# Performance work log

Measured on AMD Instinct MI355X. Metric: run time of the kernel, lower is better.

The kernel has to match this reference:

```python
import jax, jax.numpy as jnp
import numpy as np

VALUES_PER_ITEM = 4  # 2-bit packed -> 4 values per uint8


def setup_inputs() -> dict:
    key = jax.random.key(0)
    k1, k2, k3 = jax.random.split(key, 3)
    x = jax.random.normal(k1, (4, 4096, 2048), dtype=jnp.float32)
    # packed uint8 weights, stored as int32 with values in [0, 256)
    weight_packed = jax.random.randint(k2, (512, 2048), 0, 256, dtype=jnp.int32)
    weight_scale = jnp.ones((1,), dtype=jnp.float32)
    bias = jax.random.normal(k3, (2048,), dtype=jnp.float32) * 0.01
    return {"x": x, "weight_packed": weight_packed,
            "weight_scale": weight_scale, "bias": bias}


def unpack_weights_bitnet(packed, dtype):
    # packed: [out//4, in]. HF BitNet layout: group i occupies rows
    # [i*out//4 : (i+1)*out//4], extracted from bits (2i, 2i+1), minus 1.
    parts = [((packed >> (2 * i)) & 3) for i in range(VALUES_PER_ITEM)]
    return jnp.concatenate(parts, axis=0).astype(dtype) - 1.0  # [out, in]


def activation_quant(x, num_bits=8):
    qn = -(2 ** (num_bits - 1))          # -128
    qp = 2 ** (num_bits - 1) - 1         # 127
    amax = jnp.clip(jnp.max(jnp.abs(x), axis=-1, keepdims=True), 1e-5, None)
    scale = qp / amax                    # per-token scale, [..., 1]
    # round-half-to-even matches torch .round(); keep in float (int8-valued)
    xq = jnp.clip(jnp.round(x * scale), qn, qp)
    return xq, scale


def reference(x, weight_packed, weight_scale, bias):
    w = unpack_weights_bitnet(weight_packed, x.dtype)  # [out, in]
    xq, in_scale = activation_quant(x)                 # [b,s,in], [b,s,1]
    y = jnp.einsum('bsd,od->bso', xq, w)               # int8-valued GEMM in fp
    y = y / (weight_scale * in_scale)                  # rescale
    return y + bias
```

## Files before the change

### kernel.cpp

```cpp
#include <hip/hip_runtime.h>
#include <stdint.h>


typedef __attribute__((ext_vector_type(4))) int int4v;

#define GLOBAL_AS __attribute__((address_space(1)))
#define LDS_AS    __attribute__((address_space(3)))

static constexpr int MK = 2048;
static constexpr int NN = 2048;
static constexpr int MM = 16384;

__global__ void quant_kernel(const float* __restrict__ x,
                             const float* __restrict__ wscale,
                             signed char* __restrict__ xq,
                             float* __restrict__ rf) {
    const int m = blockIdx.x;
    const int t = threadIdx.x;
    const float4* xr = (const float4*)(x + (size_t)m * MK);
    float4 v0 = xr[t];
    float4 v1 = xr[t + 256];
    float amax = fmaxf(fmaxf(fabsf(v0.x), fabsf(v0.y)),
                       fmaxf(fabsf(v0.z), fabsf(v0.w)));
    amax = fmaxf(amax, fmaxf(fmaxf(fabsf(v1.x), fabsf(v1.y)),
                             fmaxf(fabsf(v1.z), fabsf(v1.w))));
    #pragma unroll
    for (int off = 32; off >= 1; off >>= 1)
        amax = fmaxf(amax, __shfl_xor(amax, off));
    __shared__ float smax[4];
    if ((t & 63) == 0) smax[t >> 6] = amax;
    __syncthreads();
    float a0 = fmaxf(fmaxf(smax[0], smax[1]), fmaxf(smax[2], smax[3]));
    a0 = fmaxf(a0, 1e-5f);
    const float scale = 127.0f / a0;
    if (t == 0) rf[m] = a0 / (127.0f * wscale[0]);

    auto q = [&](float f) -> int {
        float r = rintf(f * scale);
        r = fminf(fmaxf(r, -128.0f), 127.0f);
        return (int)r;
    };
    int p0 = (q(v0.x) & 255) | ((q(v0.y) & 255) << 8) |
             ((q(v0.z) & 255) << 16) | ((q(v0.w) & 255) << 24);
    int p1 = (q(v1.x) & 255) | ((q(v1.y) & 255) << 8) |
             ((q(v1.z) & 255) << 16) | ((q(v1.w) & 255) << 24);
    int* xqr = (int*)(xq + (size_t)m * MK);
    xqr[t]       = p0;
    xqr[t + 256] = p1;
}

__global__ void unpack_kernel(const int* __restrict__ packed,
                              signed char* __restrict__ W) {
    const int idx = blockIdx.x * 256 + threadIdx.x;
    const int r  = idx >> 9;
    const int kq = idx & 511;
    const int4 p = ((const int4*)packed)[idx];
    int* Wi = (int*)W;
    #pragma unroll
    for (int i = 0; i < 4; i++) {
        const int sh = 2 * i;
        int b0 = ((((p.x >> sh) & 3) - 1) & 255);
        int b1 = ((((p.y >> sh) & 3) - 1) & 255);
        int b2 = ((((p.z >> sh) & 3) - 1) & 255);
        int b3 = ((((p.w >> sh) & 3) - 1) & 255);
        Wi[(i * 512 + r) * 512 + kq] = b0 | (b1 << 8) | (b2 << 16) | (b3 << 24);
    }
}

#define WAITV(N) asm volatile("s_waitcnt vmcnt(" #N ")" ::: "memory")

__device__ __forceinline__ void stage_half(const signed char* __restrict__ src,
                                           int row0, int k0, int h, int ss,
                                           unsigned char* plane,
                                           int wave, int lane) {
    const int csrc = (((lane & 7) ^ (lane >> 3)) << 4);
    #pragma unroll
    for (int j = 0; j < 2; ++j) {
        const int rw = wave * 16 + j * 8 + (lane >> 3);
        const int r  = (rw & ((1 << ss) - 1)) + (h << ss)
                     + ((rw >> ss) << (ss + 1));
        const signed char* ga = src + (size_t)(row0 + r) * MK + k0 + csrc;
        __builtin_amdgcn_global_load_lds((const GLOBAL_AS void*)ga,
            (LDS_AS void*)(plane + (h << 14) + (wave * 2 + j) * 1024),
            16, 0, 0);
    }
}

#define PH(MH, NH, DO_READA, STAGE, WAIT)                                      \
  do {                                                                         \
    if (DO_READA) {                                                            \
      _Pragma("unroll")                                                        \
      for (int mt = 0; mt < 4; ++mt) {                                         \
        a[mt][0] = *(const int4v*)(shp + cb + aoff0 + (MH)*16384 + mt*2048);   \
        a[mt][1] = *(const int4v*)(shp + cb + aoff1 + (MH)*16384 + mt*2048);   \
      }                                                                        \
    }                                                                          \
    _Pragma("unroll")                                                          \
    for (int nf = 0; nf < 2; ++nf) {                                           \
      b[nf][0] = *(const int4v*)(shp + cb + boff0 + (NH)*16384 + nf*2048);     \
      b[nf][1] = *(const int4v*)(shp + cb + boff1 + (NH)*16384 + nf*2048);     \
    }                                                                          \
    STAGE;                                                                     \
    WAIT;                                                                      \
    __builtin_amdgcn_s_barrier();                                              \
    __builtin_amdgcn_sched_barrier(0);                                         \
    __builtin_amdgcn_s_setprio(1);                                             \
    _Pragma("unroll")                                                          \
    for (int mt = 0; mt < 4; ++mt) {                                           \
      _Pragma("unroll")                                                        \
      for (int nf = 0; nf < 2; ++nf) {                                         \
        acc[(MH)*4+mt][(NH)*2+nf] = __builtin_amdgcn_mfma_i32_16x16x64_i8(     \
            a[mt][0], b[nf][0], acc[(MH)*4+mt][(NH)*2+nf], 0, 0, 0);           \
        acc[(MH)*4+mt][(NH)*2+nf] = __builtin_amdgcn_mfma_i32_16x16x64_i8(     \
            a[mt][1], b[nf][1], acc[(MH)*4+mt][(NH)*2+nf], 0, 0, 0);           \
      }                                                                        \
    }                                                                          \
    __builtin_amdgcn_s_setprio(0);                                             \
  } while (0)

__global__ void __launch_bounds__(512, 2)
gemm_kernel(const signed char* __restrict__ xq,
            const signed char* __restrict__ W,
            const float* __restrict__ rf,
            const float* __restrict__ bias,
            float* __restrict__ out) {
    __shared__ __attribute__((aligned(16))) unsigned char sh[131072];
    unsigned char* shp = sh;

    const int tid  = threadIdx.x;
    const int wave = tid >> 6;
    const int lane = tid & 63;
    const int wm = wave >> 2;
    const int wn = wave & 3;

    const int bs = ((blockIdx.x & 7) << 6) | (blockIdx.x >> 3);
    const int m0 = (bs >> 3) << 8;
    const int n0 = (bs & 7) << 8;

    const int fr = lane & 15, lq = lane >> 4, f7 = fr & 7;
    const int cks0  = (lq ^ f7) << 4;
    const int aoff0 = (wm * 64 + fr) * 128 + cks0;
    const int aoff1 = aoff0 ^ 64;
    const int boff0 = 32768 + (wn * 32 + fr) * 128 + cks0;
    const int boff1 = boff0 ^ 64;

    int4v a[4][2], b[2][2];
    int4v acc[8][4] = {};

    stage_half(xq, m0, 0, 0, 6, shp,        wave, lane);
    stage_half(W,  n0, 0, 0, 5, shp + 32768, wave, lane);
    stage_half(W,  n0, 0, 1, 5, shp + 32768, wave, lane);
    stage_half(xq, m0, 0, 1, 6, shp,        wave, lane);
    WAITV(4);
    __builtin_amdgcn_s_barrier();
    __builtin_amdgcn_sched_barrier(0);

    #pragma unroll 1
    for (int t = 0; t < 15; ++t) {
        const int cb = (t & 1) << 16;
        const int nb = cb ^ 65536;
        const int k1 = (t + 1) << 7;
        PH(0, 0, 1, stage_half(xq, m0, k1, 0, 6, shp + nb,        wave, lane), WAITV(4));
        PH(0, 1, 0, stage_half(W,  n0, k1, 0, 5, shp + nb + 32768, wave, lane), WAITV(4));
        PH(1, 0, 1, stage_half(W,  n0, k1, 1, 5, shp + nb + 32768, wave, lane), WAITV(6));
        PH(1, 1, 0, stage_half(xq, m0, k1, 1, 6, shp + nb,        wave, lane), WAITV(4));
    }
    {
        const int cb = 65536;
        PH(0, 0, 1, (void)0, WAITV(2));
        PH(0, 1, 0, (void)0, WAITV(0));
        PH(1, 0, 1, (void)0, (void)0);
        PH(1, 1, 0, (void)0, (void)0);
    }

    const int col = lane & 15;
    const int rq  = (lane >> 4) * 4;
    const int nbase = n0 + wn * 64 + col;
    float bv[4];
    #pragma unroll
    for (int nf = 0; nf < 4; ++nf) bv[nf] = bias[nbase + nf * 16];
    #pragma unroll
    for (int mf = 0; mf < 8; ++mf) {
        #pragma unroll
        for (int rr = 0; rr < 4; ++rr) {
            const int m = m0 + wm * 128 + mf * 16 + rq + rr;
            const float frm = rf[m];
            float* orow = out + (size_t)m * NN;
            #pragma unroll
            for (int nf = 0; nf < 4; ++nf)
                orow[nbase + nf * 16] = (float)acc[mf][nf][rr] * frm + bv[nf];
        }
    }
}

extern "C" void kernel_launch(void* const* d_in, const int* in_sizes, int n_in,
                              void* d_out, int out_size, void* d_ws, size_t ws_size,
                              hipStream_t stream) {
    const float* x      = (const float*)d_in[0];
    const int*   packed = (const int*)d_in[1];
    const float* wscale = (const float*)d_in[2];
    const float* bias   = (const float*)d_in[3];
    float* out = (float*)d_out;

    signed char* xq = (signed char*)d_ws;
    signed char* W  = xq + (size_t)MM * MK;
    float*       rf = (float*)(W + (size_t)NN * MK);

    quant_kernel<<<MM, 256, 0, stream>>>(x, wscale, xq, rf);
    unpack_kernel<<<(512 * 512) / 256, 256, 0, stream>>>(packed, W);
    gemm_kernel<<<dim3(512), 512, 0, stream>>>(xq, W, rf, bias, out);
}
```

Measured before the change: 289.1 us.

## Switch GEMM to 32x32x32 int8 MFMA with B-fragment reuse across phases

Replaces the 16x16x64 int8 MFMA tiling with 32x32x32 int8 MFMA. Each wave now owns 4x2 tiles of 32x32, and the A/B LDS reads are reorganized so each B fragment set (b0, b1) is read once per k-step and reused across both M halves. The LDS read swizzle, the accumulator layout and the epilogue store mapping change to match. The aim is fewer LDS reads per MFMA and larger, more efficient MFMA instructions. The cost is higher register pressure from the 16-wide accumulators, and correctness depends on the new swizzle matching the staging layout.

Result: no change. 290.1 us (+0.4%).

```diff
diff --git a/kernel.cpp b/kernel.cpp
--- a/kernel.cpp
+++ b/kernel.cpp
@@ -2,7 +2,8 @@
 #include <stdint.h>
 
 
-typedef __attribute__((ext_vector_type(4))) int int4v;
+typedef __attribute__((ext_vector_type(4)))  int int4v;
+typedef __attribute__((ext_vector_type(16))) int int16v;
 
 #define GLOBAL_AS __attribute__((address_space(1)))
 #define LDS_AS    __attribute__((address_space(3)))
@@ -68,6 +69,8 @@
 }
 
 #define WAITV(N) asm volatile("s_waitcnt vmcnt(" #N ")" ::: "memory")
+#define BAR() do { __builtin_amdgcn_s_barrier(); \
+                   __builtin_amdgcn_sched_barrier(0); } while (0)
 
 __device__ __forceinline__ void stage_half(const signed char* __restrict__ src,
                                            int row0, int k0, int h, int ss,
@@ -86,35 +89,28 @@
     }
 }
 
-#define PH(MH, NH, DO_READA, STAGE, WAIT)                                      \
+#define RD_A(MH)                                                               \
+  _Pragma("unroll")                                                            \
+  for (int mt = 0; mt < 2; ++mt)                                               \
+    _Pragma("unroll")                                                          \
+    for (int ks = 0; ks < 4; ++ks)                                             \
+      a[mt][ks] = *(const int4v*)(shp + cb + (MH)*16384 + arow + mt*4096       \
+                                  + cbyte[ks]);
+
+#define RD_B(NH, breg)                                                         \
+  _Pragma("unroll")                                                            \
+  for (int ks = 0; ks < 4; ++ks)                                               \
+    breg[ks] = *(const int4v*)(shp + cb + brow + (NH)*16384 + cbyte[ks]);
+
+#define MFM(MH, NH, breg)                                                      \
   do {                                                                         \
-    if (DO_READA) {                                                            \
-      _Pragma("unroll")                                                        \
-      for (int mt = 0; mt < 4; ++mt) {                                         \
-        a[mt][0] = *(const int4v*)(shp + cb + aoff0 + (MH)*16384 + mt*2048);   \
-        a[mt][1] = *(const int4v*)(shp + cb + aoff1 + (MH)*16384 + mt*2048);   \
-      }                                                                        \
-    }                                                                          \
-    _Pragma("unroll")                                                          \
-    for (int nf = 0; nf < 2; ++nf) {                                           \
-      b[nf][0] = *(const int4v*)(shp + cb + boff0 + (NH)*16384 + nf*2048);     \
-      b[nf][1] = *(const int4v*)(shp + cb + boff1 + (NH)*16384 + nf*2048);     \
-    }                                                                          \
-    STAGE;                                                                     \
-    WAIT;                                                                      \
-    __builtin_amdgcn_s_barrier();                                              \
-    __builtin_amdgcn_sched_barrier(0);                                         \
     __builtin_amdgcn_s_setprio(1);                                             \
     _Pragma("unroll")                                                          \
-    for (int mt = 0; mt < 4; ++mt) {                                           \
+    for (int mt = 0; mt < 2; ++mt)                                             \
       _Pragma("unroll")                                                        \
-      for (int nf = 0; nf < 2; ++nf) {                                         \
-        acc[(MH)*4+mt][(NH)*2+nf] = __builtin_amdgcn_mfma_i32_16x16x64_i8(     \
-            a[mt][0], b[nf][0], acc[(MH)*4+mt][(NH)*2+nf], 0, 0, 0);           \
-        acc[(MH)*4+mt][(NH)*2+nf] = __builtin_amdgcn_mfma_i32_16x16x64_i8(     \
-            a[mt][1], b[nf][1], acc[(MH)*4+mt][(NH)*2+nf], 0, 0, 0);           \
-      }                                                                        \
-    }                                                                          \
+      for (int ks = 0; ks < 4; ++ks)                                           \
+        acc[(MH)*2+mt][NH] = __builtin_amdgcn_mfma_i32_32x32x32_i8(            \
+            a[mt][ks], breg[ks], acc[(MH)*2+mt][NH], 0, 0, 0);                 \
     __builtin_amdgcn_s_setprio(0);                                             \
   } while (0)
 
@@ -137,58 +133,86 @@
     const int m0 = (bs >> 3) << 8;
     const int n0 = (bs & 7) << 8;
 
-    const int fr = lane & 15, lq = lane >> 4, f7 = fr & 7;
-    const int cks0  = (lq ^ f7) << 4;
-    const int aoff0 = (wm * 64 + fr) * 128 + cks0;
-    const int aoff1 = aoff0 ^ 64;
-    const int boff0 = 32768 + (wn * 32 + fr) * 128 + cks0;
-    const int boff1 = boff0 ^ 64;
-
-    int4v a[4][2], b[2][2];
-    int4v acc[8][4] = {};
-
-    stage_half(xq, m0, 0, 0, 6, shp,        wave, lane);
+    const int ar = lane & 31, hl = lane >> 5;
+    int cbyte[4];
+    #pragma unroll
+    for (int ks = 0; ks < 4; ++ks)
+        cbyte[ks] = ((((ks << 1) | hl) ^ (ar & 7)) << 4);
+    const int arow = (wm * 64 + ar) * 128;
+    const int brow = 32768 + (wn * 32 + ar) * 128;
+
+    int4v a[2][4], b0[4], b1[4];
+    int16v acc[4][2] = {};
+
+    stage_half(xq, m0, 0, 0, 6, shp,         wave, lane);
     stage_half(W,  n0, 0, 0, 5, shp + 32768, wave, lane);
     stage_half(W,  n0, 0, 1, 5, shp + 32768, wave, lane);
-    stage_half(xq, m0, 0, 1, 6, shp,        wave, lane);
+    stage_half(xq, m0, 0, 1, 6, shp,         wave, lane);
     WAITV(4);
-    __builtin_amdgcn_s_barrier();
-    __builtin_amdgcn_sched_barrier(0);
+    BAR();
 
     #pragma unroll 1
     for (int t = 0; t < 15; ++t) {
         const int cb = (t & 1) << 16;
         const int nb = cb ^ 65536;
         const int k1 = (t + 1) << 7;
-        PH(0, 0, 1, stage_half(xq, m0, k1, 0, 6, shp + nb,        wave, lane), WAITV(4));
-        PH(0, 1, 0, stage_half(W,  n0, k1, 0, 5, shp + nb + 32768, wave, lane), WAITV(4));
-        PH(1, 0, 1, stage_half(W,  n0, k1, 1, 5, shp + nb + 32768, wave, lane), WAITV(6));
-        PH(1, 1, 0, stage_half(xq, m0, k1, 1, 6, shp + nb,        wave, lane), WAITV(4));
+
+        RD_A(0); RD_B(0, b0);
+        stage_half(xq, m0, k1, 0, 6, shp + nb,         wave, lane);
+        WAITV(4); BAR();
+        MFM(0, 0, b0);
+
+        RD_B(1, b1);
+        stage_half(W,  n0, k1, 0, 5, shp + nb + 32768, wave, lane);
+        WAITV(4); BAR();
+        MFM(0, 1, b1);
+
+        RD_A(1);
+        stage_half(W,  n0, k1, 1, 5, shp + nb + 32768, wave, lane);
+        WAITV(6); BAR();
+        MFM(1, 0, b0);
+
+        stage_half(xq, m0, k1, 1, 6, shp + nb,         wave, lane);
+        WAITV(4); BAR();
+        MFM(1, 1, b1);
     }
     {
         const int cb = 65536;
-        PH(0, 0, 1, (void)0, WAITV(2));
-        PH(0, 1, 0, (void)0, WAITV(0));
-        PH(1, 0, 1, (void)0, (void)0);
-        PH(1, 1, 0, (void)0, (void)0);
-    }
-
-    const int col = lane & 15;
-    const int rq  = (lane >> 4) * 4;
-    const int nbase = n0 + wn * 64 + col;
-    float bv[4];
-    #pragma unroll
-    for (int nf = 0; nf < 4; ++nf) bv[nf] = bias[nbase + nf * 16];
-    #pragma unroll
-    for (int mf = 0; mf < 8; ++mf) {
+        RD_A(0); RD_B(0, b0);
+        WAITV(2); BAR();
+        MFM(0, 0, b0);
+
+        RD_B(1, b1);
+        WAITV(0); BAR();
+        MFM(0, 1, b1);
+
+        RD_A(1);
+        BAR();
+        MFM(1, 0, b0);
+
+        BAR();
+        MFM(1, 1, b1);
+    }
+
+    const int nb0 = n0 + wn * 64 + ar;
+    const float bva = bias[nb0];
+    const float bvb = bias[nb0 + 32];
+    #pragma unroll
+    for (int MH = 0; MH < 2; ++MH) {
         #pragma unroll
-        for (int rr = 0; rr < 4; ++rr) {
-            const int m = m0 + wm * 128 + mf * 16 + rq + rr;
-            const float frm = rf[m];
-            float* orow = out + (size_t)m * NN;
+        for (int mt = 0; mt < 2; ++mt) {
+            const int mbase = m0 + wm * 128 + MH * 64 + mt * 32 + hl * 4;
             #pragma unroll
-            for (int nf = 0; nf < 4; ++nf)
-                orow[nbase + nf * 16] = (float)acc[mf][nf][rr] * frm + bv[nf];
+            for (int q = 0; q < 4; ++q) {
+                #pragma unroll
+                for (int rr = 0; rr < 4; ++rr) {
+                    const int m = mbase + q * 8 + rr;
+                    const float frm = rf[m];
+                    float* orow = out + (size_t)m * NN;
+                    orow[nb0]      = (float)acc[MH*2+mt][0][q*4+rr] * frm + bva;
+                    orow[nb0 + 32] = (float)acc[MH*2+mt][1][q*4+rr] * frm + bvb;
+                }
+            }
         }
     }
 }
```
